# Kernel optimization log

Measured on AMD Instinct MI355X. Metric: run time of the kernel, lower is better.

The kernel has to match this reference:

```python
import jax, jax.numpy as jnp
import numpy as np

TOP_K = 2

def setup_inputs() -> dict:
    key = jax.random.key(0)
    k1, k2, k3 = jax.random.split(key, 3)
    B, D, E = 32768, 768, 8
    h = jax.random.normal(k1, (B, D), dtype=jnp.float32)
    gate_w = jax.random.normal(k2, (E, D), dtype=jnp.float32) * 0.02
    gate_b = jax.random.normal(k3, (E,), dtype=jnp.float32) * 0.02
    return {"h": h, "gate_w": gate_w, "gate_b": gate_b}

def reference(h, gate_w, gate_b):
    # logits: [B, n_experts] = h @ W^T + b
    logits = jnp.einsum('bd,ed->be', h, gate_w) + gate_b
    # top-k over experts (eval path: no jitter noise)
    top_vals, indices = jax.lax.top_k(logits, TOP_K)   # [B, top_k]
    weights = jax.nn.softmax(top_vals, axis=-1)        # [B, top_k]
    return indices, weights, logits
```

## Files before the change

kernel.cpp:

```cpp
#include <hip/hip_runtime.h>
#include <hip/hip_bf16.h>
#include <math.h>


constexpr int D  = 768;
constexpr int E  = 8;
constexpr int D4 = D / 4;
constexpr int BLOCK  = 256;
constexpr int GRID_A = 1536;

__device__ __forceinline__ float dot4acc(float4 a, float4 b, float acc) {
    acc = fmaf(a.x, b.x, acc);
    acc = fmaf(a.y, b.y, acc);
    acc = fmaf(a.z, b.z, acc);
    acc = fmaf(a.w, b.w, acc);
    return acc;
}

__device__ __forceinline__ float wave_reduce8(float a[8], int lane) {
    {
        const bool hi = lane & 1;
#pragma unroll
        for (int j = 0; j < 4; ++j) {
            float send = hi ? a[j] : a[j + 4];
            float recv = __shfl_xor(send, 1, 64);
            float keep = hi ? a[j + 4] : a[j];
            a[j] = keep + recv;
        }
    }
    {
        const bool hi = lane & 2;
#pragma unroll
        for (int j = 0; j < 2; ++j) {
            float send = hi ? a[j] : a[j + 2];
            float recv = __shfl_xor(send, 2, 64);
            float keep = hi ? a[j + 2] : a[j];
            a[j] = keep + recv;
        }
    }
    {
        const bool hi = lane & 4;
        float send = hi ? a[0] : a[1];
        float recv = __shfl_xor(send, 4, 64);
        float keep = hi ? a[1] : a[0];
        a[0] = keep + recv;
    }
    float v = a[0];
    v += __shfl_xor(v, 8, 64);
    v += __shfl_xor(v, 16, 64);
    v += __shfl_xor(v, 32, 64);
    return v;
}

__global__ __launch_bounds__(BLOCK, 2)
void router_fused_kernel(const float* __restrict__ h,
                         const float* __restrict__ gate_w,
                         const float* __restrict__ gate_b,
                         float* __restrict__ out_idx,
                         float* __restrict__ out_w,
                         float* __restrict__ out_logits,
                         int B) {
    const int tid    = threadIdx.x;
    const int lane   = tid & 63;
    const int wave   = tid >> 6;
    const int gwave  = blockIdx.x * (BLOCK / 64) + wave;
    const int nwaves = gridDim.x * (BLOCK / 64);

    const int l3 = lane & 7;
    const int e_lane = ((l3 & 1) << 2) | (l3 & 2) | ((l3 >> 2) & 1);
    const float bias = gate_b[e_lane];

    __shared__ float4 gsh[E * D4];
    const float4* gw4 = (const float4*)gate_w;
#pragma unroll
    for (int i = 0; i < (E * D4) / BLOCK; ++i)
        gsh[i * BLOCK + tid] = gw4[i * BLOCK + tid];
    __syncthreads();

    const float4* h4 = (const float4*)h;

    int r = gwave;
    if (r >= B) return;

    float4 cv[3];
    {
        const float4* hp = h4 + (size_t)r * D4 + lane;
#pragma unroll
        for (int c = 0; c < 3; ++c) cv[c] = hp[c * 64];
    }

    while (true) {
        const int rn = r + nwaves;
        const bool more = (rn < B);

        float acc[E];
#pragma unroll
        for (int e = 0; e < E; ++e) acc[e] = 0.0f;
#pragma unroll
        for (int c = 0; c < 3; ++c) {
#pragma unroll
            for (int e = 0; e < E; ++e) {
                acc[e] = dot4acc(cv[c], gsh[e * D4 + c * 64 + lane], acc[e]);
            }
        }

        if (more) {
            const float4* hp = h4 + (size_t)rn * D4 + lane;
#pragma unroll
            for (int c = 0; c < 3; ++c) cv[c] = hp[c * 64];
        }

        float v = wave_reduce8(acc, lane) + bias;

        if (lane < 8) out_logits[(size_t)r * 8 + e_lane] = v;

        float t0 = v;          int x0 = e_lane;
        float t1 = -INFINITY;  int x1 = E;
#pragma unroll
        for (int m = 1; m <= 4; m <<= 1) {
            float w0 = __shfl_xor(t0, m, 64);
            int   j0 = __shfl_xor(x0, m, 64);
            float w1 = __shfl_xor(t1, m, 64);
            int   j1 = __shfl_xor(x1, m, 64);
            bool aFirst = (t0 > w0) || (t0 == w0 && x0 < j0);
            float f0  = aFirst ? t0 : w0;
            int   fi0 = aFirst ? x0 : j0;
            float losT = aFirst ? w0 : t0;
            int   losI = aFirst ? j0 : x0;
            float winT = aFirst ? t1 : w1;
            int   winI = aFirst ? x1 : j1;
            bool sWin = (winT > losT) || (winT == losT && winI < losI);
            float f1  = sWin ? winT : losT;
            int   fi1 = sWin ? winI : losI;
            t0 = f0; x0 = fi0; t1 = f1; x1 = fi1;
        }

        if (lane == 0) {
            float tt = expf(t1 - t0);
            float w0_ = 1.0f / (1.0f + tt);
            float w1_ = tt * w0_;
            ((float2*)out_idx)[r] = make_float2((float)x0, (float)x1);
            ((float2*)out_w)[r]   = make_float2(w0_, w1_);
        }

        if (!more) break;
        r = rn;
    }
}

extern "C" void kernel_launch(void* const* d_in, const int* in_sizes, int n_in,
                              void* d_out, int out_size, void* d_ws, size_t ws_size,
                              hipStream_t stream) {
    const float* h      = (const float*)d_in[0];
    const float* gate_w = (const float*)d_in[1];
    const float* gate_b = (const float*)d_in[2];

    const int B = in_sizes[0] / D;

    float* out        = (float*)d_out;
    float* out_idx    = out;
    float* out_w      = out + (size_t)B * 2;
    float* out_logits = out + (size_t)B * 4;

    router_fused_kernel<<<dim3(GRID_A), dim3(BLOCK), 0, stream>>>(
        h, gate_w, gate_b, out_idx, out_w, out_logits, B);
}
```

Measured before the change: 147.2 us.

## Process four rows per wave to reuse gate weights and share reductions

```diff
diff --git a/kernel.cpp b/kernel.cpp
--- a/kernel.cpp
+++ b/kernel.cpp
@@ -7,7 +7,7 @@
 constexpr int E  = 8;
 constexpr int D4 = D / 4;
 constexpr int BLOCK  = 256;
-constexpr int GRID_A = 1536;
+constexpr int GRID_A = 1024;
 
 __device__ __forceinline__ float dot4acc(float4 a, float4 b, float acc) {
     acc = fmaf(a.x, b.x, acc);
@@ -17,7 +17,7 @@
     return acc;
 }
 
-__device__ __forceinline__ float wave_reduce8(float a[8], int lane) {
+__device__ __forceinline__ float group_fold8(float a[8], int lane) {
     {
         const bool hi = lane & 1;
 #pragma unroll
@@ -45,11 +45,52 @@
         float keep = hi ? a[1] : a[0];
         a[0] = keep + recv;
     }
-    float v = a[0];
-    v += __shfl_xor(v, 8, 64);
-    v += __shfl_xor(v, 16, 64);
-    v += __shfl_xor(v, 32, 64);
-    return v;
+    return a[0];
+}
+
+__device__ __forceinline__ void finish_pair(float pa, float pb, float bias,
+                                            int lane, int e_lane, int rowa,
+                                            float* __restrict__ out_logits,
+                                            float* __restrict__ out_idx,
+                                            float* __restrict__ out_w) {
+    pa += __shfl_xor(pa, 8, 64);
+    pb += __shfl_xor(pb, 8, 64);
+    float q = (lane & 8) ? pb : pa;
+    q += __shfl_xor(q, 16, 64);
+    q += __shfl_xor(q, 32, 64);
+    float v = q + bias;
+
+    if (lane < 16) out_logits[(size_t)rowa * 8 + (lane & 8) + e_lane] = v;
+
+    float t0 = v;          int x0 = e_lane;
+    float t1 = -INFINITY;  int x1 = E;
+#pragma unroll
+    for (int m = 1; m <= 4; m <<= 1) {
+        float w0 = __shfl_xor(t0, m, 64);
+        int   j0 = __shfl_xor(x0, m, 64);
+        float w1 = __shfl_xor(t1, m, 64);
+        int   j1 = __shfl_xor(x1, m, 64);
+        bool aFirst = (t0 > w0) || (t0 == w0 && x0 < j0);
+        float f0  = aFirst ? t0 : w0;
+        int   fi0 = aFirst ? x0 : j0;
+        float losT = aFirst ? w0 : t0;
+        int   losI = aFirst ? j0 : x0;
+        float winT = aFirst ? t1 : w1;
+        int   winI = aFirst ? x1 : j1;
+        bool sWin = (winT > losT) || (winT == losT && winI < losI);
+        float f1  = sWin ? winT : losT;
+        int   fi1 = sWin ? winI : losI;
+        t0 = f0; x0 = fi0; t1 = f1; x1 = fi1;
+    }
+
+    if ((lane & 7) == 0 && lane < 16) {
+        float tt = expf(t1 - t0);
+        float w0_ = 1.0f / (1.0f + tt);
+        float w1_ = tt * w0_;
+        const int row = rowa + (lane >> 3);
+        ((float2*)out_idx)[row] = make_float2((float)x0, (float)x1);
+        ((float2*)out_w)[row]   = make_float2(w0_, w1_);
+    }
 }
 
 __global__ __launch_bounds__(BLOCK, 2)
@@ -78,73 +119,62 @@
     __syncthreads();
 
     const float4* h4 = (const float4*)h;
+    const int nquads = B >> 2;
 
-    int r = gwave;
-    if (r >= B) return;
+    int q = gwave;
+    if (q >= nquads) return;
 
-    float4 cv[3];
+    float4 cv[4][3];
     {
-        const float4* hp = h4 + (size_t)r * D4 + lane;
+        const float4* hp = h4 + (size_t)(4 * q) * D4 + lane;
 #pragma unroll
-        for (int c = 0; c < 3; ++c) cv[c] = hp[c * 64];
+        for (int r = 0; r < 4; ++r)
+#pragma unroll
+            for (int c = 0; c < 3; ++c)
+                cv[r][c] = hp[r * D4 + c * 64];
     }
 
     while (true) {
-        const int rn = r + nwaves;
-        const bool more = (rn < B);
+        const int qn = q + nwaves;
+        const bool more = (qn < nquads);
 
-        float acc[E];
+        float acc[4][E];
 #pragma unroll
-        for (int e = 0; e < E; ++e) acc[e] = 0.0f;
+        for (int r = 0; r < 4; ++r)
+#pragma unroll
+            for (int e = 0; e < E; ++e) acc[r][e] = 0.0f;
+
 #pragma unroll
         for (int c = 0; c < 3; ++c) {
 #pragma unroll
             for (int e = 0; e < E; ++e) {
-                acc[e] = dot4acc(cv[c], gsh[e * D4 + c * 64 + lane], acc[e]);
+                const float4 g = gsh[e * D4 + c * 64 + lane];
+#pragma unroll
+                for (int r = 0; r < 4; ++r)
+                    acc[r][e] = dot4acc(cv[r][c], g, acc[r][e]);
             }
         }
 
         if (more) {
-            const float4* hp = h4 + (size_t)rn * D4 + lane;
+            const float4* hp = h4 + (size_t)(4 * qn) * D4 + lane;
 #pragma unroll
-            for (int c = 0; c < 3; ++c) cv[c] = hp[c * 64];
+            for (int r = 0; r < 4; ++r)
+#pragma unroll
+                for (int c = 0; c < 3; ++c)
+                    cv[r][c] = hp[r * D4 + c * 64];
         }
 
-        float v = wave_reduce8(acc, lane) + bias;
+        float p0 = group_fold8(acc[0], lane);
+        float p1 = group_fold8(acc[1], lane);
+        float p2 = group_fold8(acc[2], lane);
+        float p3 = group_fold8(acc[3], lane);
 
-        if (lane < 8) out_logits[(size_t)r * 8 + e_lane] = v;
-
-        float t0 = v;          int x0 = e_lane;
-        float t1 = -INFINITY;  int x1 = E;
-#pragma unroll
-        for (int m = 1; m <= 4; m <<= 1) {
-            float w0 = __shfl_xor(t0, m, 64);
-            int   j0 = __shfl_xor(x0, m, 64);
-            float w1 = __shfl_xor(t1, m, 64);
-            int   j1 = __shfl_xor(x1, m, 64);
-            bool aFirst = (t0 > w0) || (t0 == w0 && x0 < j0);
-            float f0  = aFirst ? t0 : w0;
-            int   fi0 = aFirst ? x0 : j0;
-            float losT = aFirst ? w0 : t0;
-            int   losI = aFirst ? j0 : x0;
-            float winT = aFirst ? t1 : w1;
-            int   winI = aFirst ? x1 : j1;
-            bool sWin = (winT > losT) || (winT == losT && winI < losI);
-            float f1  = sWin ? winT : losT;
-            int   fi1 = sWin ? winI : losI;
-            t0 = f0; x0 = fi0; t1 = f1; x1 = fi1;
-        }
-
-        if (lane == 0) {
-            float tt = expf(t1 - t0);
-            float w0_ = 1.0f / (1.0f + tt);
-            float w1_ = tt * w0_;
-            ((float2*)out_idx)[r] = make_float2((float)x0, (float)x1);
-            ((float2*)out_w)[r]   = make_float2(w0_, w1_);
-        }
+        const int rbase = 4 * q;
+        finish_pair(p0, p1, bias, lane, e_lane, rbase,     out_logits, out_idx, out_w);
+        finish_pair(p2, p3, bias, lane, e_lane, rbase + 2, out_logits, out_idx, out_w);
 
         if (!more) break;
-        r = rn;
+        q = qn;
     }
 }
 
```

Result: no change. 148.4 us (+0.8%).
